# Optimization experiments

Measured on AMD Instinct MI355X. Metric: run time of the kernel, lower is better.

## Reference

```python
import jax, jax.numpy as jnp
import numpy as np

N = 50000   # nodes
E = 800000  # edges
C = 64      # node feature channels (0e)
A = 4       # edge attr channels
B = 16      # edge embedding (radial basis) size
H = 8       # radial MLP hidden size
D = 32      # query/key channels
P = 16      # node attr channels
R_MAX = 5.0


def setup_inputs() -> dict:
    key = jax.random.key(0)
    ks = jax.random.split(key, 20)
    w = lambda k, shape, fan_in: (jax.random.normal(k, shape, jnp.float32) / np.sqrt(fan_in).astype(np.float32))
    inp = {
        "node_feats": jax.random.normal(ks[0], (N, C), jnp.float32),
        "node_attrs": jax.random.normal(ks[1], (N, P), jnp.float32),
        "edge_embedding": jax.random.uniform(ks[2], (E, B), jnp.float32),
        "edge_attrs": jax.random.normal(ks[3], (E, A), jnp.float32),
        "positions": jax.random.normal(ks[4], (N, 3), jnp.float32) * 0.3,  # keep lengths < r_max
        "edge_src": jax.random.randint(ks[5], (E,), 0, N),
        "edge_dst": jax.random.randint(ks[6], (E,), 0, N),
        # parameters
        "W_q": w(ks[7], (C, D), C),            # h_q Linear
        "W1_k": w(ks[8], (B, H), B),           # radial MLP for tp_k
        "W2_k": w(ks[9], (H, C * A), H),
        "W1_v": w(ks[10], (B, H), B),          # radial MLP for tp_v
        "W2_v": w(ks[11], (H, C * A), H),
        "W_lin_k": w(ks[12], (C, D), C),       # linear_k
        "W_lin_v": w(ks[13], (C, C), C),       # linear_v
        "W_dot": w(ks[14], (D, D), D * D),     # FullyConnectedTensorProduct(q,k,'0e')
        "W_sc": w(ks[15], (C, P, C), C * P),   # self connection FCTP
    }
    return inp


def soft_unit_step(x):
    safe = jnp.where(x > 0, x, 1.0)
    return jnp.where(x > 0, jnp.exp(-1.0 / safe), 0.0)


def uvu_tp(x_src, edge_attrs, edge_embedding, W1, W2):
    # radial MLP -> per-edge, per-path weights [E, C, A]; 'uvu' tensor product on scalars
    wgt = (jax.nn.silu(edge_embedding @ W1) @ W2).reshape(-1, C, A)
    return x_src * (jnp.einsum('eca,ea->ec', wgt, edge_attrs) / np.sqrt(A).astype(np.float32))


def reference(node_feats, node_attrs, edge_embedding, edge_attrs, positions,
              edge_src, edge_dst, W_q, W1_k, W2_k, W1_v, W2_v,
              W_lin_k, W_lin_v, W_dot, W_sc):
    q = (node_feats @ W_q)[edge_dst]                              # [E, D]
    x_src = node_feats[edge_src]                                  # [E, C]
    k = uvu_tp(x_src, edge_attrs, edge_embedding, W1_k, W2_k) @ W_lin_k  # [E, D]
    v = uvu_tp(x_src, edge_attrs, edge_embedding, W1_v, W2_v) @ W_lin_v  # [E, C]

    edge_vec = positions[edge_dst] - positions[edge_src]
    edge_length = jnp.linalg.norm(edge_vec, axis=1)               # [E]
    cutoff = soft_unit_step(2.0 * R_MAX * (1.0 - edge_length / R_MAX))

    score = jnp.einsum('ei,ij,ej->e', q, W_dot, k)                # weighted bilinear dot -> 0e
    expv = cutoff * jnp.exp(score)                                # [E]
    z = jax.ops.segment_sum(expv, edge_dst, num_segments=N)       # softmax normalizer
    z = jnp.where(z == 0, 1.0, z)
    alpha = expv / z[edge_dst]
    msg = jnp.sqrt(jax.nn.relu(alpha))[:, None] * v               # [E, C]
    node_out = jax.ops.segment_sum(msg, edge_dst, num_segments=N)  # [N, C]

    sc = jnp.einsum('nc,np,cpo->no', node_feats, node_attrs, W_sc)
    return node_out + sc
```

## Files before the change

kernel.cpp:

```cpp
#include <hip/hip_runtime.h>
#include <math.h>

#define NN 50000
#define EE 800000
#define NPAD 50176
#define CPAD 66

typedef __attribute__((ext_vector_type(8))) short short8v;
typedef __attribute__((ext_vector_type(4))) float f32x4;

static __device__ __forceinline__ short bf16r(float x) {
  union { float f; unsigned u; } v; v.f = x;
  unsigned r = v.u + 0x7FFFu + ((v.u >> 16) & 1u);
  return (short)(r >> 16);
}
static __device__ __forceinline__ float bf2f(unsigned u) {
  union { unsigned u; float f; } v; v.u = u << 16;
  return v.f;
}


__global__ __launch_bounds__(256) void fold_kernel(
    const float* __restrict__ Wq, const float* __restrict__ Wdot,
    const float* __restrict__ Wlk, const float* __restrict__ W2k,
    const float* __restrict__ W2v, const float* __restrict__ Wlv,
    float* __restrict__ M, unsigned short* __restrict__ w2kT,
    unsigned short* __restrict__ w2vT, unsigned short* __restrict__ wlvb)
{
  __shared__ float tmp[2048];
  const int tid = threadIdx.x;
#pragma unroll
  for (int r = 0; r < 8; ++r) {
    int idx = tid + r * 256;
    int cin = idx >> 5, d = idx & 31;
    float a = 0.f;
    for (int j = 0; j < 32; ++j) a = fmaf(Wq[cin * 32 + j], Wdot[j * 32 + d], a);
    tmp[idx] = a;
  }
  __syncthreads();
#pragma unroll
  for (int r = 0; r < 16; ++r) {
    int idx = tid + r * 256;
    int cin = idx >> 6, c = idx & 63;
    float a = 0.f;
    for (int d = 0; d < 32; ++d) a = fmaf(tmp[cin * 32 + d], Wlk[c * 32 + d], a);
    M[idx] = a;
  }
#pragma unroll
  for (int r = 0; r < 8; ++r) {
    int idx = tid + r * 256;
    int c = idx >> 5, k = idx & 31, h = k >> 2, a = k & 3;
    w2kT[idx] = (unsigned short)bf16r(W2k[h * 256 + c * 4 + a]);
    w2vT[idx] = (unsigned short)bf16r(W2v[h * 256 + c * 4 + a]);
  }
#pragma unroll
  for (int r = 0; r < 16; ++r) {
    int idx = tid + r * 256;
    int o = idx >> 6, c = idx & 63;
    wlvb[idx] = (unsigned short)bf16r(Wlv[c * 64 + o]);
  }
}

__global__ __launch_bounds__(256) void prep_wsc(
    const float* __restrict__ Wsc, unsigned short* __restrict__ wscb)
{
  int w = blockIdx.x * 256 + threadIdx.x;
  int c = w & 63, o = (w >> 6) & 63, p = w >> 12;
  wscb[w] = (unsigned short)bf16r(Wsc[c * 1024 + p * 64 + o]);
}

__global__ __launch_bounds__(256) void hist_kernel(
    const int* __restrict__ edst, int* __restrict__ cnt)
{
  int e = blockIdx.x * 256 + threadIdx.x;
  atomicAdd(&cnt[edst[e]], 1);
}

__global__ __launch_bounds__(256) void scanA_kernel(
    const int* __restrict__ cnt, int* __restrict__ start, int* __restrict__ bsum)
{
  __shared__ int s[256];
  const int tid = threadIdx.x;
  const int i = blockIdx.x * 256 + tid;
  int v = cnt[i];
  s[tid] = v;
  __syncthreads();
  for (int off = 1; off < 256; off <<= 1) {
    int t = (tid >= off) ? s[tid - off] : 0;
    __syncthreads();
    s[tid] += t;
    __syncthreads();
  }
  start[i] = s[tid] - v;
  if (tid == 255) bsum[blockIdx.x] = s[255];
}

__global__ __launch_bounds__(256) void scanB_kernel(int* __restrict__ bsum)
{
  __shared__ int s[256];
  const int tid = threadIdx.x;
  int v = (tid < 196) ? bsum[tid] : 0;
  s[tid] = v;
  __syncthreads();
  for (int off = 1; off < 256; off <<= 1) {
    int t = (tid >= off) ? s[tid - off] : 0;
    __syncthreads();
    s[tid] += t;
    __syncthreads();
  }
  if (tid < 196) bsum[tid] = s[tid] - v;
}

__global__ __launch_bounds__(256) void scanC_kernel(
    int* __restrict__ start, const int* __restrict__ bsum, int* __restrict__ cur)
{
  const int i = blockIdx.x * 256 + threadIdx.x;
  int sv = start[i] + bsum[blockIdx.x];
  start[i] = sv;
  cur[i] = sv;
}

__global__ __launch_bounds__(256) void scatter_fused(
    const int* __restrict__ esrc, const int* __restrict__ edst,
    const float* __restrict__ ea, const float* __restrict__ eb,
    const float* __restrict__ pos, const float* __restrict__ W1k,
    const float* __restrict__ W1v, int* __restrict__ cur,
    int* __restrict__ ssrc, int* __restrict__ sdst, float* __restrict__ scl,
    float4* __restrict__ sea, unsigned short* __restrict__ hwb)
{
  int e = blockIdx.x * 256 + threadIdx.x;
  int s = esrc[e], d = edst[e];
  int r = atomicAdd(&cur[d], 1);
  ssrc[r] = s;
  sdst[r] = d;
  sea[r] = reinterpret_cast<const float4*>(ea)[e];
  float dx = pos[d * 3 + 0] - pos[s * 3 + 0];
  float dy = pos[d * 3 + 1] - pos[s * 3 + 1];
  float dz = pos[d * 3 + 2] - pos[s * 3 + 2];
  float len = sqrtf(fmaf(dx, dx, fmaf(dy, dy, dz * dz)));
  float arg = 10.f - 2.f * len;
  scl[r] = (arg > 0.f) ? __expf(-1.f / arg) : 0.f;
  const float4* eb4 = reinterpret_cast<const float4*>(eb);
  float4 q0 = eb4[e * 4 + 0], q1 = eb4[e * 4 + 1],
         q2 = eb4[e * 4 + 2], q3 = eb4[e * 4 + 3];
  float ebv[16] = {q0.x, q0.y, q0.z, q0.w, q1.x, q1.y, q1.z, q1.w,
                   q2.x, q2.y, q2.z, q2.w, q3.x, q3.y, q3.z, q3.w};
  float h[16];
#pragma unroll
  for (int j = 0; j < 16; ++j) h[j] = 0.f;
#pragma unroll
  for (int b = 0; b < 16; ++b) {
    float x = ebv[b];
#pragma unroll
    for (int j = 0; j < 8; ++j) {
      h[j]     = fmaf(x, W1k[b * 8 + j], h[j]);
      h[8 + j] = fmaf(x, W1v[b * 8 + j], h[8 + j]);
    }
  }
  short8v pk, pv;
#pragma unroll
  for (int j = 0; j < 8; ++j) {
    float a = h[j]     / (1.f + __expf(-h[j]));
    float b = h[8 + j] / (1.f + __expf(-h[8 + j]));
    pk[j] = bf16r(a);
    pv[j] = bf16r(b);
  }
  *reinterpret_cast<short8v*>(&hwb[(size_t)r * 16]) = pk;
  *reinterpret_cast<short8v*>(&hwb[(size_t)r * 16 + 8]) = pv;
}

__global__ __launch_bounds__(256) void tq_kernel(
    const float* __restrict__ nf, const float* __restrict__ M, float* __restrict__ tq)
{
  __shared__ float Ml[4096];
  __shared__ float nfl[64 * 68];
  const int tid = threadIdx.x;
  const int base = blockIdx.x * 64;
#pragma unroll
  for (int r = 0; r < 4; ++r) {
    int idx = tid + r * 256;
    reinterpret_cast<float4*>(Ml)[idx] = reinterpret_cast<const float4*>(M)[idx];
  }
#pragma unroll
  for (int r = 0; r < 4; ++r) {
    int idx = tid + r * 256;
    int row = idx >> 4, c4 = idx & 15;
    float4 v = make_float4(0.f, 0.f, 0.f, 0.f);
    if (base + row < NN) v = reinterpret_cast<const float4*>(nf)[(base + row) * 16 + c4];
    *reinterpret_cast<float4*>(&nfl[row * 68 + c4 * 4]) = v;
  }
  __syncthreads();
  const int to = tid & 15, tn = tid >> 4;
  float4 acc[4] = {make_float4(0,0,0,0), make_float4(0,0,0,0),
                   make_float4(0,0,0,0), make_float4(0,0,0,0)};
  for (int c = 0; c < 64; ++c) {
    float4 m = reinterpret_cast<const float4*>(Ml)[c * 16 + to];
#pragma unroll
    for (int i = 0; i < 4; ++i) {
      float x = nfl[(tn * 4 + i) * 68 + c];
      acc[i].x = fmaf(x, m.x, acc[i].x);
      acc[i].y = fmaf(x, m.y, acc[i].y);
      acc[i].z = fmaf(x, m.z, acc[i].z);
      acc[i].w = fmaf(x, m.w, acc[i].w);
    }
  }
#pragma unroll
  for (int i = 0; i < 4; ++i) {
    int n = base + tn * 4 + i;
    if (n < NN) reinterpret_cast<float4*>(tq)[n * 16 + to] = acc[i];
  }
}

__global__ __launch_bounds__(256) void edge_kernel(
    const float* __restrict__ nf, const float* __restrict__ tq,
    const int* __restrict__ ssrc, const int* __restrict__ sdst,
    const float* __restrict__ scl, const float4* __restrict__ sea,
    const unsigned short* __restrict__ hwb,
    const unsigned short* __restrict__ w2kT, const unsigned short* __restrict__ w2vT,
    float* __restrict__ z, float* __restrict__ U)
{
  __shared__ float ys[64 * CPAD];
  __shared__ float xs[64 * CPAD];
  __shared__ int   ed[64];
  __shared__ float cl[64];
  __shared__ float evs[64];
  const int tid  = threadIdx.x;
  const int lane = tid & 63;
  const int lo = lane & 15, hi = lane >> 4;
  const int w = tid >> 6;
  const int sb = blockIdx.x * 64;
  const int row = 16 * w + lo;

  short8v bk[4], bv[4];
#pragma unroll
  for (int t = 0; t < 4; ++t) {
    bk[t] = *reinterpret_cast<const short8v*>(&w2kT[(16 * t + lo) * 32 + hi * 8]);
    bv[t] = *reinterpret_cast<const short8v*>(&w2vT[(16 * t + lo) * 32 + hi * 8]);
  }
  const unsigned short* hwp = &hwb[(size_t)(sb + row) * 16];
  unsigned k01 = *reinterpret_cast<const unsigned*>(&hwp[2 * hi]);
  unsigned v01 = *reinterpret_cast<const unsigned*>(&hwp[8 + 2 * hi]);
  float4 a4 = sea[sb + row];

  if (tid < 64) {
    ed[tid] = sdst[sb + tid];
    cl[tid] = scl[sb + tid];
  }
#pragma unroll
  for (int r = 0; r < 4; ++r) {
    int idx = tid + r * 256;
    int e = idx >> 4, c4 = idx & 15;
    int s = ssrc[sb + e], d = sdst[sb + e];
    float4 xv = reinterpret_cast<const float4*>(nf)[s * 16 + c4];
    float4 tv = reinterpret_cast<const float4*>(tq)[d * 16 + c4];
    float* xp = &xs[e * CPAD + c4 * 4];
    xp[0] = xv.x; xp[1] = xv.y; xp[2] = xv.z; xp[3] = xv.w;
    float* yp = &ys[e * CPAD + c4 * 4];
    yp[0] = xv.x * tv.x; yp[1] = xv.y * tv.y; yp[2] = xv.z * tv.z; yp[3] = xv.w * tv.w;
  }

  float hk0 = bf2f(k01 & 0xffffu), hk1 = bf2f(k01 >> 16);
  float hv0 = bf2f(v01 & 0xffffu), hv1 = bf2f(v01 >> 16);
  short8v ak, av;
  ak[0] = bf16r(hk0 * a4.x); ak[1] = bf16r(hk0 * a4.y);
  ak[2] = bf16r(hk0 * a4.z); ak[3] = bf16r(hk0 * a4.w);
  ak[4] = bf16r(hk1 * a4.x); ak[5] = bf16r(hk1 * a4.y);
  ak[6] = bf16r(hk1 * a4.z); ak[7] = bf16r(hk1 * a4.w);
  av[0] = bf16r(hv0 * a4.x); av[1] = bf16r(hv0 * a4.y);
  av[2] = bf16r(hv0 * a4.z); av[3] = bf16r(hv0 * a4.w);
  av[4] = bf16r(hv1 * a4.x); av[5] = bf16r(hv1 * a4.y);
  av[6] = bf16r(hv1 * a4.z); av[7] = bf16r(hv1 * a4.w);

  __syncthreads();

  f32x4 zero = {0.f, 0.f, 0.f, 0.f};
  f32x4 ack[4], acv[4];
#pragma unroll
  for (int t = 0; t < 4; ++t) {
    ack[t] = __builtin_amdgcn_mfma_f32_16x16x32_bf16(ak, bk[t], zero, 0, 0, 0);
    acv[t] = __builtin_amdgcn_mfma_f32_16x16x32_bf16(av, bv[t], zero, 0, 0, 0);
  }

  const int erow = 16 * w + 4 * hi;
  float p0, p1, p2, p3;
  {
    const float* y0 = &ys[(erow + 0) * CPAD + lo];
    const float* y1 = &ys[(erow + 1) * CPAD + lo];
    const float* y2 = &ys[(erow + 2) * CPAD + lo];
    const float* y3 = &ys[(erow + 3) * CPAD + lo];
    p0 = y0[0]*ack[0][0] + y0[16]*ack[1][0] + y0[32]*ack[2][0] + y0[48]*ack[3][0];
    p1 = y1[0]*ack[0][1] + y1[16]*ack[1][1] + y1[32]*ack[2][1] + y1[48]*ack[3][1];
    p2 = y2[0]*ack[0][2] + y2[16]*ack[1][2] + y2[32]*ack[2][2] + y2[48]*ack[3][2];
    p3 = y3[0]*ack[0][3] + y3[16]*ack[1][3] + y3[32]*ack[2][3] + y3[48]*ack[3][3];
  }
#pragma unroll
  for (int off = 1; off < 16; off <<= 1) {
    p0 += __shfl_xor(p0, off);
    p1 += __shfl_xor(p1, off);
    p2 += __shfl_xor(p2, off);
    p3 += __shfl_xor(p3, off);
  }
  float ev0 = cl[erow + 0] * __expf(0.5f * p0);
  float ev1 = cl[erow + 1] * __expf(0.5f * p1);
  float ev2 = cl[erow + 2] * __expf(0.5f * p2);
  float ev3 = cl[erow + 3] * __expf(0.5f * p3);
  float se0 = sqrtf(ev0), se1 = sqrtf(ev1), se2 = sqrtf(ev2), se3 = sqrtf(ev3);
  if (lo < 4) {
    float ev = (lo == 0) ? ev0 : (lo == 1) ? ev1 : (lo == 2) ? ev2 : ev3;
    evs[erow + lo] = ev;
  }
#pragma unroll
  for (int i = 0; i < 4; ++i) {
    const float se = (i == 0) ? se0 : (i == 1) ? se1 : (i == 2) ? se2 : se3;
    float* mr = &ys[(erow + i) * CPAD + lo];
    const float* xr = &xs[(erow + i) * CPAD + lo];
#pragma unroll
    for (int t = 0; t < 4; ++t) {
      mr[16 * t] = se * xr[16 * t] * acv[t][i];
    }
  }
  {
    const int c = lane;
    float acc = 0.f, evacc = 0.f;
    int prev = ed[16 * w];
    for (int r = 16 * w; r < 16 * w + 16; ++r) {
      int d = ed[r];
      if (d != prev) {
        unsafeAtomicAdd(&U[prev * 64 + c], acc);
        if (c == 0) unsafeAtomicAdd(&z[prev], evacc);
        acc = 0.f; evacc = 0.f; prev = d;
      }
      acc += ys[r * CPAD + c];
      if (c == 0) evacc += evs[r];
    }
    unsafeAtomicAdd(&U[prev * 64 + c], acc);
    if (c == 0) unsafeAtomicAdd(&z[prev], evacc);
  }
}

__global__ __launch_bounds__(256) void final_kernel(
    const float* __restrict__ nf, const float* __restrict__ na,
    const float* __restrict__ U, const float* __restrict__ z,
    const unsigned short* __restrict__ wscb, const unsigned short* __restrict__ wlvb,
    float* __restrict__ out)
{
  __shared__ float nfl[64 * 68];
  __shared__ float Ul[64 * 68];
  __shared__ float nal[64 * 17];
  __shared__ float sl[64];
  const int tid = threadIdx.x;
  const int lane = tid & 63;
  const int lo = lane & 15, hi = lane >> 4;
  const int w = tid >> 6;
  const int nb = blockIdx.x * 64;

#pragma unroll
  for (int r = 0; r < 4; ++r) {
    int idx = tid + r * 256;
    int row = idx >> 4, c4 = idx & 15;
    int n = nb + row; if (n >= NN) n = NN - 1;
    float4 v = reinterpret_cast<const float4*>(nf)[n * 16 + c4];
    *reinterpret_cast<float4*>(&nfl[row * 68 + c4 * 4]) = v;
    float4 u = reinterpret_cast<const float4*>(U)[n * 16 + c4];
    *reinterpret_cast<float4*>(&Ul[row * 68 + c4 * 4]) = u;
  }
#pragma unroll
  for (int r = 0; r < 4; ++r) {
    int idx = tid + r * 256;
    int row = idx >> 4, p = idx & 15;
    int n = nb + row; if (n >= NN) n = NN - 1;
    nal[row * 17 + p] = na[n * 16 + p];
  }
  if (tid < 64) {
    int n = nb + tid; if (n >= NN) n = NN - 1;
    float zz = z[n];
    sl[tid] = (zz > 0.f) ? 0.5f * rsqrtf(zz) : 0.f;
  }
  __syncthreads();

  const int row = 16 * w + lo;
  short8v anf[2], au[2];
#pragma unroll
  for (int kk = 0; kk < 2; ++kk) {
#pragma unroll
    for (int j = 0; j < 8; ++j) {
      anf[kk][j] = bf16r(nfl[row * 68 + 32 * kk + 8 * hi + j]);
      au[kk][j]  = bf16r(Ul[row * 68 + 32 * kk + 8 * hi + j]);
    }
  }

  f32x4 zeroA = {0.f, 0.f, 0.f, 0.f};
  f32x4 accS[4] = {zeroA, zeroA, zeroA, zeroA};
  f32x4 accU[4] = {zeroA, zeroA, zeroA, zeroA};

#pragma unroll
  for (int t = 0; t < 4; ++t) {
    short8v b0 = *reinterpret_cast<const short8v*>(&wlvb[(16 * t + lo) * 64 + 8 * hi]);
    short8v b1 = *reinterpret_cast<const short8v*>(&wlvb[(16 * t + lo) * 64 + 32 + 8 * hi]);
    accU[t] = __builtin_amdgcn_mfma_f32_16x16x32_bf16(au[0], b0, accU[t], 0, 0, 0);
    accU[t] = __builtin_amdgcn_mfma_f32_16x16x32_bf16(au[1], b1, accU[t], 0, 0, 0);
  }
  for (int p = 0; p < 16; ++p) {
    f32x4 cp[4] = {zeroA, zeroA, zeroA, zeroA};
#pragma unroll
    for (int t = 0; t < 4; ++t) {
      const int bbase = (p * 64 + 16 * t + lo) * 64 + 8 * hi;
      short8v b0 = *reinterpret_cast<const short8v*>(&wscb[bbase]);
      short8v b1 = *reinterpret_cast<const short8v*>(&wscb[bbase + 32]);
      cp[t] = __builtin_amdgcn_mfma_f32_16x16x32_bf16(anf[0], b0, cp[t], 0, 0, 0);
      cp[t] = __builtin_amdgcn_mfma_f32_16x16x32_bf16(anf[1], b1, cp[t], 0, 0, 0);
    }
#pragma unroll
    for (int i = 0; i < 4; ++i) {
      float nav = nal[(16 * w + 4 * hi + i) * 17 + p];
#pragma unroll
      for (int t = 0; t < 4; ++t) accS[t][i] = fmaf(nav, cp[t][i], accS[t][i]);
    }
  }
#pragma unroll
  for (int i = 0; i < 4; ++i) {
    int n = nb + 16 * w + 4 * hi + i;
    if (n < NN) {
      float s = sl[16 * w + 4 * hi + i];
#pragma unroll
      for (int t = 0; t < 4; ++t) {
        out[n * 64 + 16 * t + lo] = fmaf(s, accU[t][i], accS[t][i]);
      }
    }
  }
}

extern "C" void kernel_launch(void* const* d_in, const int* in_sizes, int n_in,
                              void* d_out, int out_size, void* d_ws, size_t ws_size,
                              hipStream_t stream) {
  const float* nf   = (const float*)d_in[0];
  const float* na   = (const float*)d_in[1];
  const float* eb   = (const float*)d_in[2];
  const float* ea   = (const float*)d_in[3];
  const float* pos  = (const float*)d_in[4];
  const int*   esrc = (const int*)d_in[5];
  const int*   edst = (const int*)d_in[6];
  const float* Wq   = (const float*)d_in[7];
  const float* W1k  = (const float*)d_in[8];
  const float* W2k  = (const float*)d_in[9];
  const float* W1v  = (const float*)d_in[10];
  const float* W2v  = (const float*)d_in[11];
  const float* Wlk  = (const float*)d_in[12];
  const float* Wlv  = (const float*)d_in[13];
  const float* Wdot = (const float*)d_in[14];
  const float* Wsc  = (const float*)d_in[15];
  float* out = (float*)d_out;

  float* wsf = (float*)d_ws;
  float* z     = wsf;
  float* U     = wsf + 65536;
  int*   cnt   = (int*)(wsf + 3265536);
  int*   start = (int*)(wsf + 3315712);
  int*   cur   = (int*)(wsf + 3365888);
  int*   bsum  = (int*)(wsf + 3416064);
  float* tq    = wsf + 3416320;
  float* M     = wsf + 6616320;
  unsigned short* w2kT = (unsigned short*)(wsf + 6620416);
  unsigned short* w2vT = (unsigned short*)(wsf + 6621440);
  unsigned short* wlvb = (unsigned short*)(wsf + 6622464);
  unsigned short* wscb = (unsigned short*)(wsf + 6624512);
  int*   ssrc  = (int*)(wsf + 6657280);
  int*   sdst  = (int*)(wsf + 7457280);
  float* scl   = wsf + 8257280;
  float4* sea  = (float4*)(wsf + 9057280);
  unsigned short* hwb = (unsigned short*)(wsf + 12257280);

  hipMemsetAsync(z, 0, (size_t)(3265536 + NPAD) * sizeof(float), stream);

  fold_kernel<<<1, 256, 0, stream>>>(Wq, Wdot, Wlk, W2k, W2v, Wlv, M, w2kT, w2vT, wlvb);
  prep_wsc<<<256, 256, 0, stream>>>(Wsc, wscb);
  hist_kernel<<<EE / 256, 256, 0, stream>>>(edst, cnt);
  scanA_kernel<<<NPAD / 256, 256, 0, stream>>>(cnt, start, bsum);
  scanB_kernel<<<1, 256, 0, stream>>>(bsum);
  scanC_kernel<<<NPAD / 256, 256, 0, stream>>>(start, bsum, cur);
  scatter_fused<<<EE / 256, 256, 0, stream>>>(esrc, edst, ea, eb, pos, W1k, W1v,
                                              cur, ssrc, sdst, scl, sea, hwb);
  tq_kernel<<<(NN + 63) / 64, 256, 0, stream>>>(nf, M, tq);
  edge_kernel<<<EE / 64, 256, 0, stream>>>(nf, tq, ssrc, sdst, scl, sea, hwb,
                                           w2kT, w2vT, z, U);
  final_kernel<<<(NN + 63) / 64, 256, 0, stream>>>(nf, na, U, z, wscb, wlvb, out);
}
```

Measured before the change: 350.9 us.

## Pack sorted per-edge data into one 64-byte record and alias workspace buffers

The scatter kernel now writes source, destination, cutoff, edge attrs and the bf16 hidden radial activations into a single 16-float record per sorted edge. This replaces five separate scattered arrays, so each edge becomes one full-line write, and the edge kernel reads everything from one contiguous record. The workspace is also compacted: the counters, M and tq share space with U and wscb, and launches are reordered so the aliased buffers are consumed before being overwritten. The reordering relies on strict stream ordering and slightly raises the per-edge stored bytes through padding.

```diff
diff --git a/kernel.cpp b/kernel.cpp
--- a/kernel.cpp
+++ b/kernel.cpp
@@ -17,6 +17,9 @@
 static __device__ __forceinline__ float bf2f(unsigned u) {
   union { unsigned u; float f; } v; v.u = u << 16;
   return v.f;
+}
+static __device__ __forceinline__ unsigned pk2(float a, float b) {
+  return (unsigned)(unsigned short)bf16r(a) | ((unsigned)(unsigned short)bf16r(b) << 16);
 }
 
 
@@ -70,19 +73,19 @@
 }
 
 __global__ __launch_bounds__(256) void hist_kernel(
-    const int* __restrict__ edst, int* __restrict__ cnt)
+    const int* __restrict__ edst, int* __restrict__ cur)
 {
   int e = blockIdx.x * 256 + threadIdx.x;
-  atomicAdd(&cnt[edst[e]], 1);
+  atomicAdd(&cur[edst[e]], 1);
 }
 
 __global__ __launch_bounds__(256) void scanA_kernel(
-    const int* __restrict__ cnt, int* __restrict__ start, int* __restrict__ bsum)
+    int* __restrict__ cur, int* __restrict__ bsum)
 {
   __shared__ int s[256];
   const int tid = threadIdx.x;
   const int i = blockIdx.x * 256 + tid;
-  int v = cnt[i];
+  int v = cur[i];
   s[tid] = v;
   __syncthreads();
   for (int off = 1; off < 256; off <<= 1) {
@@ -91,7 +94,7 @@
     s[tid] += t;
     __syncthreads();
   }
-  start[i] = s[tid] - v;
+  cur[i] = s[tid] - v;
   if (tid == 255) bsum[blockIdx.x] = s[255];
 }
 
@@ -112,12 +115,10 @@
 }
 
 __global__ __launch_bounds__(256) void scanC_kernel(
-    int* __restrict__ start, const int* __restrict__ bsum, int* __restrict__ cur)
+    int* __restrict__ cur, const int* __restrict__ bsum)
 {
   const int i = blockIdx.x * 256 + threadIdx.x;
-  int sv = start[i] + bsum[blockIdx.x];
-  start[i] = sv;
-  cur[i] = sv;
+  cur[i] += bsum[blockIdx.x];
 }
 
 __global__ __launch_bounds__(256) void scatter_fused(
@@ -125,21 +126,17 @@
     const float* __restrict__ ea, const float* __restrict__ eb,
     const float* __restrict__ pos, const float* __restrict__ W1k,
     const float* __restrict__ W1v, int* __restrict__ cur,
-    int* __restrict__ ssrc, int* __restrict__ sdst, float* __restrict__ scl,
-    float4* __restrict__ sea, unsigned short* __restrict__ hwb)
+    float* __restrict__ rec)
 {
   int e = blockIdx.x * 256 + threadIdx.x;
   int s = esrc[e], d = edst[e];
   int r = atomicAdd(&cur[d], 1);
-  ssrc[r] = s;
-  sdst[r] = d;
-  sea[r] = reinterpret_cast<const float4*>(ea)[e];
   float dx = pos[d * 3 + 0] - pos[s * 3 + 0];
   float dy = pos[d * 3 + 1] - pos[s * 3 + 1];
   float dz = pos[d * 3 + 2] - pos[s * 3 + 2];
   float len = sqrtf(fmaf(dx, dx, fmaf(dy, dy, dz * dz)));
   float arg = 10.f - 2.f * len;
-  scl[r] = (arg > 0.f) ? __expf(-1.f / arg) : 0.f;
+  float cl = (arg > 0.f) ? __expf(-1.f / arg) : 0.f;
   const float4* eb4 = reinterpret_cast<const float4*>(eb);
   float4 q0 = eb4[e * 4 + 0], q1 = eb4[e * 4 + 1],
          q2 = eb4[e * 4 + 2], q3 = eb4[e * 4 + 3];
@@ -157,16 +154,25 @@
       h[8 + j] = fmaf(x, W1v[b * 8 + j], h[8 + j]);
     }
   }
-  short8v pk, pv;
-#pragma unroll
-  for (int j = 0; j < 8; ++j) {
-    float a = h[j]     / (1.f + __expf(-h[j]));
-    float b = h[8 + j] / (1.f + __expf(-h[8 + j]));
-    pk[j] = bf16r(a);
-    pv[j] = bf16r(b);
-  }
-  *reinterpret_cast<short8v*>(&hwb[(size_t)r * 16]) = pk;
-  *reinterpret_cast<short8v*>(&hwb[(size_t)r * 16 + 8]) = pv;
+#pragma unroll
+  for (int j = 0; j < 16; ++j) h[j] = h[j] / (1.f + __expf(-h[j]));
+
+  float* rp = rec + (size_t)r * 16;
+  float4 w0;
+  w0.x = __int_as_float(s); w0.y = __int_as_float(d); w0.z = cl; w0.w = 0.f;
+  reinterpret_cast<float4*>(rp)[0] = w0;
+  reinterpret_cast<float4*>(rp)[1] = reinterpret_cast<const float4*>(ea)[e];
+  float4 w2, w3;
+  w2.x = __uint_as_float(pk2(h[0], h[1]));
+  w2.y = __uint_as_float(pk2(h[2], h[3]));
+  w2.z = __uint_as_float(pk2(h[4], h[5]));
+  w2.w = __uint_as_float(pk2(h[6], h[7]));
+  w3.x = __uint_as_float(pk2(h[8], h[9]));
+  w3.y = __uint_as_float(pk2(h[10], h[11]));
+  w3.z = __uint_as_float(pk2(h[12], h[13]));
+  w3.w = __uint_as_float(pk2(h[14], h[15]));
+  reinterpret_cast<float4*>(rp)[2] = w2;
+  reinterpret_cast<float4*>(rp)[3] = w3;
 }
 
 __global__ __launch_bounds__(256) void tq_kernel(
@@ -213,9 +219,7 @@
 
 __global__ __launch_bounds__(256) void edge_kernel(
     const float* __restrict__ nf, const float* __restrict__ tq,
-    const int* __restrict__ ssrc, const int* __restrict__ sdst,
-    const float* __restrict__ scl, const float4* __restrict__ sea,
-    const unsigned short* __restrict__ hwb,
+    const float* __restrict__ rec,
     const unsigned short* __restrict__ w2kT, const unsigned short* __restrict__ w2vT,
     float* __restrict__ z, float* __restrict__ U)
 {
@@ -237,20 +241,24 @@
     bk[t] = *reinterpret_cast<const short8v*>(&w2kT[(16 * t + lo) * 32 + hi * 8]);
     bv[t] = *reinterpret_cast<const short8v*>(&w2vT[(16 * t + lo) * 32 + hi * 8]);
   }
-  const unsigned short* hwp = &hwb[(size_t)(sb + row) * 16];
-  unsigned k01 = *reinterpret_cast<const unsigned*>(&hwp[2 * hi]);
-  unsigned v01 = *reinterpret_cast<const unsigned*>(&hwp[8 + 2 * hi]);
-  float4 a4 = sea[sb + row];
+  const unsigned* ru = reinterpret_cast<const unsigned*>(rec);
+  const size_t rb = (size_t)(sb + row) * 16;
+  unsigned k01 = ru[rb + 8 + hi];
+  unsigned v01 = ru[rb + 12 + hi];
+  float4 a4 = *reinterpret_cast<const float4*>(rec + rb + 4);
 
   if (tid < 64) {
-    ed[tid] = sdst[sb + tid];
-    cl[tid] = scl[sb + tid];
+    const size_t rb2 = (size_t)(sb + tid) * 16;
+    ed[tid] = (int)ru[rb2 + 1];
+    cl[tid] = rec[rb2 + 2];
   }
 #pragma unroll
   for (int r = 0; r < 4; ++r) {
     int idx = tid + r * 256;
     int e = idx >> 4, c4 = idx & 15;
-    int s = ssrc[sb + e], d = sdst[sb + e];
+    const size_t rb3 = (size_t)(sb + e) * 16;
+    int s = (int)ru[rb3 + 0];
+    int d = (int)ru[rb3 + 1];
     float4 xv = reinterpret_cast<const float4*>(nf)[s * 16 + c4];
     float4 tv = reinterpret_cast<const float4*>(tq)[d * 16 + c4];
     float* xp = &xs[e * CPAD + c4 * 4];
@@ -452,36 +460,28 @@
   float* out = (float*)d_out;
 
   float* wsf = (float*)d_ws;
-  float* z     = wsf;
-  float* U     = wsf + 65536;
-  int*   cnt   = (int*)(wsf + 3265536);
-  int*   start = (int*)(wsf + 3315712);
-  int*   cur   = (int*)(wsf + 3365888);
-  int*   bsum  = (int*)(wsf + 3416064);
-  float* tq    = wsf + 3416320;
-  float* M     = wsf + 6616320;
-  unsigned short* w2kT = (unsigned short*)(wsf + 6620416);
-  unsigned short* w2vT = (unsigned short*)(wsf + 6621440);
-  unsigned short* wlvb = (unsigned short*)(wsf + 6622464);
-  unsigned short* wscb = (unsigned short*)(wsf + 6624512);
-  int*   ssrc  = (int*)(wsf + 6657280);
-  int*   sdst  = (int*)(wsf + 7457280);
-  float* scl   = wsf + 8257280;
-  float4* sea  = (float4*)(wsf + 9057280);
-  unsigned short* hwb = (unsigned short*)(wsf + 12257280);
-
-  hipMemsetAsync(z, 0, (size_t)(3265536 + NPAD) * sizeof(float), stream);
+  float* z    = wsf;
+  float* U    = wsf + 50176;
+  int*   cur  = (int*)(wsf + 50176);
+  int*   bsum = (int*)(wsf + 100352);
+  float* M    = wsf + 100608;
+  float* tq   = wsf + 3250176;
+  unsigned short* wscb = (unsigned short*)(wsf + 3250176);
+  unsigned short* w2kT = (unsigned short*)(wsf + 6450176);
+  unsigned short* w2vT = (unsigned short*)(wsf + 6451200);
+  unsigned short* wlvb = (unsigned short*)(wsf + 6452224);
+  float* rec  = wsf + 6454272;
 
   fold_kernel<<<1, 256, 0, stream>>>(Wq, Wdot, Wlk, W2k, W2v, Wlv, M, w2kT, w2vT, wlvb);
+  tq_kernel<<<(NN + 63) / 64, 256, 0, stream>>>(nf, M, tq);
+  hipMemsetAsync(cur, 0, (size_t)(NPAD + 256) * sizeof(int), stream);
+  hist_kernel<<<EE / 256, 256, 0, stream>>>(edst, cur);
+  scanA_kernel<<<NPAD / 256, 256, 0, stream>>>(cur, bsum);
+  scanB_kernel<<<1, 256, 0, stream>>>(bsum);
+  scanC_kernel<<<NPAD / 256, 256, 0, stream>>>(cur, bsum);
+  scatter_fused<<<EE / 256, 256, 0, stream>>>(esrc, edst, ea, eb, pos, W1k, W1v, cur, rec);
+  hipMemsetAsync(z, 0, (size_t)3250176 * sizeof(float), stream);
+  edge_kernel<<<EE / 64, 256, 0, stream>>>(nf, tq, rec, w2kT, w2vT, z, U);
   prep_wsc<<<256, 256, 0, stream>>>(Wsc, wscb);
-  hist_kernel<<<EE / 256, 256, 0, stream>>>(edst, cnt);
-  scanA_kernel<<<NPAD / 256, 256, 0, stream>>>(cnt, start, bsum);
-  scanB_kernel<<<1, 256, 0, stream>>>(bsum);
-  scanC_kernel<<<NPAD / 256, 256, 0, stream>>>(start, bsum, cur);
-  scatter_fused<<<EE / 256, 256, 0, stream>>>(esrc, edst, ea, eb, pos, W1k, W1v,
-                                              cur, ssrc, sdst, scl, sea, hwb);
-  tq_kernel<<<(NN + 63) / 64, 256, 0, stream>>>(nf, M, tq);
-  edge_kernel<<<EE / 64, 256, 0, stream>>>(nf, tq, ssrc, sdst, scl, sea, hwb,
-                                           w2kT, w2vT, z, U);
   final_kernel<<<(NN + 63) / 64, 256, 0, stream>>>(nf, na, U, z, wscb, wlvb, out);
 }
```

Result: faster. 330.0 us (-6.0%).
